# Kernel tuning notes

Hardware: AMD Instinct MI355X
Metric: run time of the kernel (lower is better)

Reference implementation:

```python
import jax, jax.numpy as jnp
import numpy as np

EMB = 2048
N_HEADS = 16
HEAD_DIM = 128
N_KV = 4
ROPE_BASE = 10000.0
B, S = 2, 2048


def _rope(x, cos, sin):
    # x: [B,S,h,d]; cos/sin: [1,S,1,d//2]
    x1, x2 = x[..., ::2], x[..., 1::2]
    return jnp.concatenate([x1 * cos - x2 * sin, x1 * sin + x2 * cos], axis=-1)


def setup_inputs() -> dict:
    key = jax.random.key(0)
    ks = jax.random.split(key, 5)
    x = jax.random.normal(ks[0], (B, S, EMB), dtype=jnp.float32)
    wq = jax.random.normal(ks[1], (EMB, N_HEADS * HEAD_DIM), dtype=jnp.float32) * 0.02
    wk = jax.random.normal(ks[2], (EMB, N_KV * HEAD_DIM), dtype=jnp.float32) * 0.02
    wv = jax.random.normal(ks[3], (EMB, N_KV * HEAD_DIM), dtype=jnp.float32) * 0.02
    wo = jax.random.normal(ks[4], (N_HEADS * HEAD_DIM, EMB), dtype=jnp.float32) * 0.02
    mask = jnp.tril(jnp.ones((S, S), dtype=bool))[None, None]  # [1,1,S,S] causal
    return {"x": x, "wq": wq, "wk": wk, "wv": wv, "wo": wo, "mask": mask}


def reference(x, wq, wk, wv, wo, mask):
    b, s, _ = x.shape
    q = (x @ wq).reshape(b, s, N_HEADS, HEAD_DIM)
    k = (x @ wk).reshape(b, s, N_KV, HEAD_DIM)
    v = (x @ wv).reshape(b, s, N_KV, HEAD_DIM)

    pos = jnp.arange(s, dtype=jnp.float32)
    dim_range = jnp.arange(0, HEAD_DIM, 2, dtype=jnp.float32)
    freqs = 1.0 / ROPE_BASE ** (dim_range / HEAD_DIM)
    angles = pos[:, None] * freqs[None, :]            # [S, d/2]
    cos = jnp.cos(angles)[None, :, None, :]           # [1,S,1,d/2]
    sin = jnp.sin(angles)[None, :, None, :]

    q = _rope(q, cos, sin)
    k = _rope(k, cos, sin)

    rep = N_HEADS // N_KV
    k = jnp.tile(k, (1, 1, rep, 1))  # matches torch .repeat on group dim
    v = jnp.tile(v, (1, 1, rep, 1))

    scale = 1.0 / jnp.sqrt(jnp.float32(HEAD_DIM))
    scores = jnp.einsum('bqhd,bkhd->bhqk', q, k) * scale  # [B,H,S,S]
    scores = jnp.where(mask, scores, -jnp.inf)
    attn = jax.nn.softmax(scores, axis=-1)  # dropout is identity in eval
    out = jnp.einsum('bhqk,bkhd->bqhd', attn, v).reshape(b, s, N_HEADS * HEAD_DIM)
    return out @ wo
```

## Files before the change

### kernel.cpp

```cpp
#include <hip/hip_runtime.h>

#define EMB 2048
#define NH 16
#define NKV 4
#define HD 128
#define SLEN 2048
#define BSZ 2
#define MROWS (BSZ * SLEN)

#define QOFF (BSZ * NH * SLEN * HD)
#define KOFF (BSZ * NKV * SLEN * HD)

typedef __attribute__((ext_vector_type(8))) short bf16x8;
typedef __attribute__((ext_vector_type(4))) float f32x4;
typedef __attribute__((ext_vector_type(2))) float f32x2;
typedef __attribute__((ext_vector_type(4))) short s16x4;

__device__ __forceinline__ short f2bf(float f) {
  union { float f; unsigned u; } v; v.f = f;
  unsigned r = (v.u + 0x7fffu + ((v.u >> 16) & 1u)) >> 16;
  return (short)r;
}

__global__ void rope_tab_k(f32x2* __restrict__ tab) {
  int i = blockIdx.x * blockDim.x + threadIdx.x;
  if (i >= SLEN * 64) return;
  int s = i >> 6, j = i & 63;
  float freq = exp2f(-(float)j * (13.287712379549449f / 64.0f));
  float ang = (float)s * freq;
  float sv, cv;
  sincosf(ang, &sv, &cv);
  f32x2 cs; cs[0] = cv; cs[1] = sv;
  tab[i] = cs;
}

__global__ void cast_bf16_k(const float* __restrict__ in, short* __restrict__ outp, int n) {
  int i = (blockIdx.x * blockDim.x + threadIdx.x) * 4;
  if (i >= n) return;
  f32x4 v = *(const f32x4*)(in + i);
  s16x4 r;
#pragma unroll
  for (int k = 0; k < 4; ++k) r[k] = f2bf(v[k]);
  *(s16x4*)(outp + i) = r;
}

__global__ void transpose_cast_k(const float* __restrict__ in, short* __restrict__ outp,
                                 int R, int C) {
  __shared__ float t[32][33];
  int c0 = blockIdx.x * 32, r0 = blockIdx.y * 32;
  int tx = threadIdx.x, ty = threadIdx.y;
#pragma unroll
  for (int i = 0; i < 4; ++i)
    t[ty + i * 8][tx] = in[(size_t)(r0 + ty + i * 8) * C + (c0 + tx)];
  __syncthreads();
#pragma unroll
  for (int i = 0; i < 4; ++i)
    outp[(size_t)(c0 + ty + i * 8) * R + (r0 + tx)] = f2bf(t[tx][ty + i * 8]);
}

#define BM 128
#define BN 128
#define BK 32

#define GLL16(g, l)                                                        \
  __builtin_amdgcn_global_load_lds(                                        \
      (const __attribute__((address_space(1))) void*)(g),                  \
      (__attribute__((address_space(3))) void*)(l), 16, 0, 0)

template <int EPI>
__global__ __launch_bounds__(256, 2) void gemm_bt_k(
    const short* __restrict__ A, const short* __restrict__ Bt,
    float* __restrict__ Cf, short* __restrict__ Cb,
    int M, int N, int K, const f32x2* __restrict__ rope) {
  __shared__ short lA[2][BM * BK];
  __shared__ short lB[2][BN * BK];
  int tid = threadIdx.x;
  int lane = tid & 63, wid = tid >> 6;
  int m0 = blockIdx.y * BM, n0 = blockIdx.x * BN;
  int wr = (wid >> 1) * 64, wc = (wid & 1) * 64;
  int l16 = lane & 15, lk = (lane >> 4) * 8;
  (void)M;

  auto stage = [&](int buf, int k0) {
    const short* ga = A + (size_t)m0 * K + k0;
    const short* gb = Bt + (size_t)n0 * K + k0;
#pragma unroll
    for (int i = 0; i < 2; ++i) {
      int cidx = i * 256 + tid;
      int row = cidx >> 2, c8 = (cidx & 3) << 3;
      GLL16(ga + (size_t)row * K + c8, &lA[buf][(size_t)(i * 256 + (tid & 192)) * 8]);
      GLL16(gb + (size_t)row * K + c8, &lB[buf][(size_t)(i * 256 + (tid & 192)) * 8]);
    }
  };

  f32x4 acc[4][4] = {};
  stage(0, 0);
  asm volatile("s_waitcnt vmcnt(0)" ::: "memory");
  __syncthreads();
  int nk = K / BK;
  for (int t = 0; t < nk; ++t) {
    int buf = t & 1;
    if (t + 1 < nk) stage(buf ^ 1, (t + 1) * BK);
    bf16x8 af[4], bfv[4];
#pragma unroll
    for (int m = 0; m < 4; ++m)
      af[m] = *(const bf16x8*)&lA[buf][(wr + m * 16 + l16) * BK + lk];
#pragma unroll
    for (int n = 0; n < 4; ++n)
      bfv[n] = *(const bf16x8*)&lB[buf][(wc + n * 16 + l16) * BK + lk];
#pragma unroll
    for (int m = 0; m < 4; ++m)
#pragma unroll
      for (int n = 0; n < 4; ++n)
        acc[m][n] = __builtin_amdgcn_mfma_f32_16x16x32_bf16(af[m], bfv[n], acc[m][n], 0, 0, 0);
    asm volatile("s_waitcnt vmcnt(0)" ::: "memory");
    __syncthreads();
  }

  const float SCL2E = 0.08838834764831845f * 1.4426950408889634f;
#pragma unroll
  for (int m = 0; m < 4; ++m) {
#pragma unroll
    for (int n = 0; n < 4; ++n) {
#pragma unroll
      for (int j = 0; j < 4; ++j) {
        int gm = m0 + wr + m * 16 + (lane >> 4) * 4 + j;
        int gc = n0 + wc + n * 16 + l16;
        float v = acc[m][n][j];
        if constexpr (EPI == 0) {
          Cf[(size_t)gm * N + gc] = v;
        } else {
          int pos = gm & (SLEN - 1), bb = gm >> 11;
          if (gc < 2560) {
            float p = __shfl_xor(v, 1);
            bool isq = gc < 2048;
            int gcc = isq ? gc : gc - 2048;
            int head = gcc >> 7, d = gcc & 127, j2 = d >> 1;
            f32x2 cs = rope[pos * 64 + j2];
            float ov; int od;
            if ((d & 1) == 0) { ov = v * cs[0] - p * cs[1]; od = j2; }
            else              { ov = p * cs[1] + v * cs[0]; od = j2 + 64; }
            if (isq) ov *= SCL2E;
            size_t idx = isq
                ? (((size_t)(bb * NH + head) * SLEN + pos) * HD + od)
                : ((size_t)QOFF + ((size_t)(bb * NKV + head) * SLEN + pos) * HD + od);
            Cb[idx] = f2bf(ov);
          } else {
            int gcc = gc - 2560;
            int head = gcc >> 7, d = gcc & 127;
            Cb[(size_t)QOFF + KOFF + ((size_t)(bb * NKV + head) * HD + d) * SLEN + pos] = f2bf(v);
          }
        }
      }
    }
  }
}

__global__ __launch_bounds__(512, 2) void flash_k(
    const short* __restrict__ Qb, const short* __restrict__ Kb,
    const short* __restrict__ Vt, short* __restrict__ O) {
  __shared__ short lK[4][64 * 128];
  __shared__ short lV[4][128 * 64];
  __shared__ short Plds[8][16][64];

  int tid = threadIdx.x, lane = tid & 63, wid = tid >> 6;
  int bh = blockIdx.y;
  int b = bh >> 4, h = bh & 15, kv = h & 3;
  int l16 = lane & 15, lk4 = lane >> 4;
  int qtA = 15 - (int)blockIdx.x;
  int qtB = (int)blockIdx.x;
  int ntA = 2 * (qtA + 1);
  int ntot = ntA + 2 * (qtB + 1);

  const short* qptr = Qb + (size_t)(b * NH + h) * SLEN * HD;
  const char* kg = (const char*)(Kb + (size_t)(b * NKV + kv) * SLEN * HD);
  const char* vg = (const char*)(Vt + (size_t)(b * NKV + kv) * HD * SLEN);

  int qbw = qtA * 128 + wid * 16;
  bf16x8 aq[4];
#pragma unroll
  for (int c = 0; c < 4; ++c)
    aq[c] = *(const bf16x8*)(qptr + (size_t)(qbw + l16) * HD + c * 32 + lk4 * 8);

  f32x4 o[8] = {};
  float m = -__builtin_inff();
  float lsum = 0.0f;

  char* myP = (char*)&Plds[wid][0][0];
  int swz = (l16 & 7) << 4;
  int swzk = l16 << 4;

  auto stageKV = [&](int buf, int k0) {
#pragma unroll
    for (int r = 0; r < 2; ++r) {
      int X = tid * 16 + r * 8192;
      int row = X >> 8, cb = X & 255;
      GLL16(kg + (size_t)(k0 + row) * 256 + (cb ^ ((row & 15) << 4)),
            (char*)&lK[buf][0] + X);
    }
#pragma unroll
    for (int r = 0; r < 2; ++r) {
      int X = tid * 16 + r * 8192;
      int row = X >> 7, cb = X & 127;
      GLL16(vg + (size_t)row * (SLEN * 2) + k0 * 2 + (cb ^ ((row & 7) << 4)),
            (char*)&lV[buf][0] + X);
    }
  };
  auto k0_of = [&](int t) { return (t < ntA ? t : t - ntA) * 64; };

  auto finalize = [&]() {
    float ls = lsum;
    ls += __shfl_xor(ls, 16);
    ls += __shfl_xor(ls, 32);
    float inv = 1.0f / ls;
    size_t ro = ((size_t)(b * SLEN + qbw + l16)) * (NH * HD) + h * HD;
#pragma unroll
    for (int dt = 0; dt < 8; ++dt) {
      s16x4 r;
#pragma unroll
      for (int j = 0; j < 4; ++j) r[j] = f2bf(o[dt][j] * inv);
      *(s16x4*)(O + ro + dt * 16 + lk4 * 4) = r;
    }
  };

  stageKV(0, k0_of(0));
  stageKV(1, k0_of(1));
  stageKV(2, k0_of(2));

  for (int tt = 0; tt < ntot; ++tt) {
    int rem = ntot - 1 - tt;
    if (rem >= 2)      asm volatile("s_waitcnt vmcnt(8)" ::: "memory");
    else if (rem == 1) asm volatile("s_waitcnt vmcnt(4)" ::: "memory");
    else               asm volatile("s_waitcnt vmcnt(0)" ::: "memory");
    __builtin_amdgcn_s_barrier();
    __builtin_amdgcn_sched_barrier(0);

    if (tt == ntA) {
      finalize();
#pragma unroll
      for (int dt = 0; dt < 8; ++dt) o[dt] = (f32x4){0.f, 0.f, 0.f, 0.f};
      m = -__builtin_inff();
      lsum = 0.0f;
      qbw = qtB * 128 + wid * 16;
#pragma unroll
      for (int c = 0; c < 4; ++c)
        aq[c] = *(const bf16x8*)(qptr + (size_t)(qbw + l16) * HD + c * 32 + lk4 * 8);
    }

    int k0 = k0_of(tt);
    int buf = tt & 3;
    if (k0 < qbw + 16) {
      const char* Kbase = (const char*)&lK[buf][0];
      const char* Vbase = (const char*)&lV[buf][0];
      f32x4 s[4] = {};
      __builtin_amdgcn_s_setprio(1);
#pragma unroll
      for (int c = 0; c < 4; ++c) {
#pragma unroll
        for (int t = 0; t < 4; ++t) {
          bf16x8 bk = *(const bf16x8*)(Kbase + (t * 16 + l16) * 256 + ((c * 64 + lk4 * 16) ^ swzk));
          s[t] = __builtin_amdgcn_mfma_f32_16x16x32_bf16(bk, aq[c], s[t], 0, 0, 0);
        }
      }
      __builtin_amdgcn_s_setprio(0);
      float x[16];
#pragma unroll
      for (int t = 0; t < 4; ++t)
#pragma unroll
        for (int j = 0; j < 4; ++j) x[t * 4 + j] = s[t][j];
      if (k0 + 63 > qbw) {
        int kq = k0 + lk4 * 4 - qbw - l16;
#pragma unroll
        for (int t = 0; t < 4; ++t)
#pragma unroll
          for (int j = 0; j < 4; ++j)
            if (kq + t * 16 + j > 0) x[t * 4 + j] = -3.0e38f;
      }
      float a0 = fmaxf(x[0], x[1]), a1 = fmaxf(x[2], x[3]);
      float a2 = fmaxf(x[4], x[5]), a3 = fmaxf(x[6], x[7]);
      float a4 = fmaxf(x[8], x[9]), a5 = fmaxf(x[10], x[11]);
      float a6 = fmaxf(x[12], x[13]), a7 = fmaxf(x[14], x[15]);
      float b0 = fmaxf(fmaxf(a0, a1), fmaxf(a2, a3));
      float b1 = fmaxf(fmaxf(a4, a5), fmaxf(a6, a7));
      float tm = fmaxf(b0, b1);
      tm = fmaxf(tm, __shfl_xor(tm, 16));
      tm = fmaxf(tm, __shfl_xor(tm, 32));
      float mn = fmaxf(m, tm);
      if (!__all(tm <= m + 8.0f)) {
        float f = __builtin_amdgcn_exp2f(m - mn);
        m = mn;
        lsum *= f;
#pragma unroll
        for (int dt = 0; dt < 8; ++dt) o[dt] *= f;
      }
      float psum = 0.0f;
#pragma unroll
      for (int t = 0; t < 4; ++t) {
        float p0 = __builtin_amdgcn_exp2f(x[t * 4 + 0] - m);
        float p1 = __builtin_amdgcn_exp2f(x[t * 4 + 1] - m);
        float p2 = __builtin_amdgcn_exp2f(x[t * 4 + 2] - m);
        float p3 = __builtin_amdgcn_exp2f(x[t * 4 + 3] - m);
        psum += (p0 + p1) + (p2 + p3);
        unsigned lo, hi;
        asm("v_cvt_pk_bf16_f32 %0, %1, %2" : "=v"(lo) : "v"(p0), "v"(p1));
        asm("v_cvt_pk_bf16_f32 %0, %1, %2" : "=v"(hi) : "v"(p2), "v"(p3));
        unsigned long long dw = ((unsigned long long)hi << 32) | lo;
        *(unsigned long long*)(myP + ((l16 * 128 + t * 32 + lk4 * 8) ^ swz)) = dw;
      }
      lsum += psum;
      asm volatile("s_waitcnt lgkmcnt(0)" ::: "memory");
      __builtin_amdgcn_sched_barrier(0);
      __builtin_amdgcn_s_setprio(1);
#pragma unroll
      for (int hh = 0; hh < 2; ++hh) {
        bf16x8 pa = *(const bf16x8*)(myP + ((l16 * 128 + hh * 64 + lk4 * 16) ^ swz));
#pragma unroll
        for (int dt = 0; dt < 8; ++dt) {
          bf16x8 bv = *(const bf16x8*)(Vbase + (dt * 16 + l16) * 128 + ((hh * 64 + lk4 * 16) ^ swz));
          o[dt] = __builtin_amdgcn_mfma_f32_16x16x32_bf16(bv, pa, o[dt], 0, 0, 0);
        }
      }
      __builtin_amdgcn_s_setprio(0);
    }
    if (tt + 3 < ntot) stageKV((tt + 3) & 3, k0_of(tt + 3));
  }
  finalize();
}

extern "C" void kernel_launch(void* const* d_in, const int* in_sizes, int n_in,
                              void* d_out, int out_size, void* d_ws, size_t ws_size,
                              hipStream_t stream) {
  const float* x  = (const float*)d_in[0];
  const float* wq = (const float*)d_in[1];
  const float* wk = (const float*)d_in[2];
  const float* wv = (const float*)d_in[3];
  const float* wo = (const float*)d_in[4];
  float* out = (float*)d_out;
  char* ws = (char*)d_ws;
  (void)in_sizes; (void)n_in; (void)out_size; (void)ws_size;

  const size_t MB = 1024 * 1024;
  f32x2* rope   = (f32x2*)(ws);
  short* xb     = (short*)(ws + 1 * MB);
  short* wqkvT  = (short*)(ws + 17 * MB);
  short* woT    = (short*)(ws + 29 * MB);
  short* QKVb   = (short*)(ws + 37 * MB);
  short* O      = xb;

  short* Qb = QKVb;
  short* Kb = QKVb + QOFF;
  short* Vt = QKVb + QOFF + KOFF;

  rope_tab_k<<<(SLEN * 64 + 255) / 256, 256, 0, stream>>>(rope);
  cast_bf16_k<<<(MROWS * EMB / 4 + 255) / 256, 256, 0, stream>>>(x, xb, MROWS * EMB);

  dim3 tb(32, 8);
  transpose_cast_k<<<dim3(2048 / 32, 2048 / 32), tb, 0, stream>>>(wq, wqkvT, 2048, 2048);
  transpose_cast_k<<<dim3(512 / 32, 2048 / 32), tb, 0, stream>>>(wk, wqkvT + 2048 * 2048, 2048, 512);
  transpose_cast_k<<<dim3(512 / 32, 2048 / 32), tb, 0, stream>>>(wv, wqkvT + 2560 * 2048, 2048, 512);
  transpose_cast_k<<<dim3(2048 / 32, 2048 / 32), tb, 0, stream>>>(wo, woT, 2048, 2048);

  gemm_bt_k<5><<<dim3(3072 / BN, MROWS / BM), 256, 0, stream>>>(xb, wqkvT, nullptr, QKVb, MROWS, 3072, 2048, rope);

  flash_k<<<dim3(8, BSZ * NH), 512, 0, stream>>>(Qb, Kb, Vt, O);

  gemm_bt_k<0><<<dim3(2048 / BN, MROWS / BM), 256, 0, stream>>>(O, woT, out, nullptr, MROWS, 2048, 2048, rope);
}
```

Baseline: 215.8 us.

## Use XOR-swizzled LDS tiles with BK=64 in the GEMM and raise MFMA priority

Doubles the GEMM K-tile to 64, halving the barrier and wait iterations per output tile. Stores A/B tiles in LDS with an XOR swizzle on 16-byte chunks to avoid bank conflicts on the fragment reads. Wraps each MFMA block in s_setprio so matrix work is issued ahead of other waves. It also drops the RoPE half-split reordering and writes Q/K in interleaved order, which is valid because the permutation is identical for Q and K. The larger tiles double LDS use per block, which may limit occupancy.

```diff
diff --git a/kernel.cpp b/kernel.cpp
--- a/kernel.cpp
+++ b/kernel.cpp
@@ -58,10 +58,6 @@
     outp[(size_t)(c0 + ty + i * 8) * R + (r0 + tx)] = f2bf(t[tx][ty + i * 8]);
 }
 
-#define BM 128
-#define BN 128
-#define BK 32
-
 #define GLL16(g, l)                                                        \
   __builtin_amdgcn_global_load_lds(                                        \
       (const __attribute__((address_space(1))) void*)(g),                  \
@@ -72,47 +68,60 @@
     const short* __restrict__ A, const short* __restrict__ Bt,
     float* __restrict__ Cf, short* __restrict__ Cb,
     int M, int N, int K, const f32x2* __restrict__ rope) {
-  __shared__ short lA[2][BM * BK];
-  __shared__ short lB[2][BN * BK];
+  __shared__ short lA[2][128 * 64];
+  __shared__ short lB[2][128 * 64];
   int tid = threadIdx.x;
   int lane = tid & 63, wid = tid >> 6;
-  int m0 = blockIdx.y * BM, n0 = blockIdx.x * BN;
+  int m0 = blockIdx.y * 128, n0 = blockIdx.x * 128;
   int wr = (wid >> 1) * 64, wc = (wid & 1) * 64;
-  int l16 = lane & 15, lk = (lane >> 4) * 8;
+  int l16 = lane & 15, lk4 = lane >> 4;
+  const int K2B = K * 2;
+  const char* Ab = (const char*)A;
+  const char* Bb = (const char*)Bt;
   (void)M;
 
   auto stage = [&](int buf, int k0) {
-    const short* ga = A + (size_t)m0 * K + k0;
-    const short* gb = Bt + (size_t)n0 * K + k0;
-#pragma unroll
-    for (int i = 0; i < 2; ++i) {
-      int cidx = i * 256 + tid;
-      int row = cidx >> 2, c8 = (cidx & 3) << 3;
-      GLL16(ga + (size_t)row * K + c8, &lA[buf][(size_t)(i * 256 + (tid & 192)) * 8]);
-      GLL16(gb + (size_t)row * K + c8, &lB[buf][(size_t)(i * 256 + (tid & 192)) * 8]);
-    }
+#pragma unroll
+    for (int r = 0; r < 4; ++r) {
+      int X = tid * 16 + r * 4096;
+      int row = X >> 7, cb = X & 127;
+      int logical = cb ^ ((row & 7) << 4);
+      GLL16(Ab + (size_t)(m0 + row) * K2B + k0 * 2 + logical, (char*)&lA[buf][0] + X);
+      GLL16(Bb + (size_t)(n0 + row) * K2B + k0 * 2 + logical, (char*)&lB[buf][0] + X);
+    }
+  };
+  auto ldA = [&](int buf, int m, int kk) {
+    int row = wr + m * 16 + l16;
+    return *(const bf16x8*)((char*)&lA[buf][0] + row * 128 + ((kk * 64 + lk4 * 16) ^ ((row & 7) << 4)));
+  };
+  auto ldB = [&](int buf, int n, int kk) {
+    int row = wc + n * 16 + l16;
+    return *(const bf16x8*)((char*)&lB[buf][0] + row * 128 + ((kk * 64 + lk4 * 16) ^ ((row & 7) << 4)));
   };
 
   f32x4 acc[4][4] = {};
   stage(0, 0);
   asm volatile("s_waitcnt vmcnt(0)" ::: "memory");
   __syncthreads();
-  int nk = K / BK;
+  int nk = K / 64;
   for (int t = 0; t < nk; ++t) {
     int buf = t & 1;
-    if (t + 1 < nk) stage(buf ^ 1, (t + 1) * BK);
-    bf16x8 af[4], bfv[4];
-#pragma unroll
-    for (int m = 0; m < 4; ++m)
-      af[m] = *(const bf16x8*)&lA[buf][(wr + m * 16 + l16) * BK + lk];
-#pragma unroll
-    for (int n = 0; n < 4; ++n)
-      bfv[n] = *(const bf16x8*)&lB[buf][(wc + n * 16 + l16) * BK + lk];
-#pragma unroll
-    for (int m = 0; m < 4; ++m)
-#pragma unroll
-      for (int n = 0; n < 4; ++n)
-        acc[m][n] = __builtin_amdgcn_mfma_f32_16x16x32_bf16(af[m], bfv[n], acc[m][n], 0, 0, 0);
+    if (t + 1 < nk) stage(buf ^ 1, (t + 1) * 64);
+#pragma unroll
+    for (int kk = 0; kk < 2; ++kk) {
+      bf16x8 af[4], bfv[4];
+#pragma unroll
+      for (int m = 0; m < 4; ++m) af[m] = ldA(buf, m, kk);
+#pragma unroll
+      for (int n = 0; n < 4; ++n) bfv[n] = ldB(buf, n, kk);
+      __builtin_amdgcn_s_setprio(1);
+#pragma unroll
+      for (int m = 0; m < 4; ++m)
+#pragma unroll
+        for (int n = 0; n < 4; ++n)
+          acc[m][n] = __builtin_amdgcn_mfma_f32_16x16x32_bf16(af[m], bfv[n], acc[m][n], 0, 0, 0);
+      __builtin_amdgcn_s_setprio(0);
+    }
     asm volatile("s_waitcnt vmcnt(0)" ::: "memory");
     __syncthreads();
   }
@@ -124,7 +133,7 @@
     for (int n = 0; n < 4; ++n) {
 #pragma unroll
       for (int j = 0; j < 4; ++j) {
-        int gm = m0 + wr + m * 16 + (lane >> 4) * 4 + j;
+        int gm = m0 + wr + m * 16 + lk4 * 4 + j;
         int gc = n0 + wc + n * 16 + l16;
         float v = acc[m][n][j];
         if constexpr (EPI == 0) {
@@ -135,15 +144,14 @@
             float p = __shfl_xor(v, 1);
             bool isq = gc < 2048;
             int gcc = isq ? gc : gc - 2048;
-            int head = gcc >> 7, d = gcc & 127, j2 = d >> 1;
-            f32x2 cs = rope[pos * 64 + j2];
-            float ov; int od;
-            if ((d & 1) == 0) { ov = v * cs[0] - p * cs[1]; od = j2; }
-            else              { ov = p * cs[1] + v * cs[0]; od = j2 + 64; }
+            int head = gcc >> 7, d = gcc & 127;
+            f32x2 cs = rope[pos * 64 + (d >> 1)];
+            float ov = ((d & 1) == 0) ? (v * cs[0] - p * cs[1])
+                                      : (p * cs[1] + v * cs[0]);
             if (isq) ov *= SCL2E;
             size_t idx = isq
-                ? (((size_t)(bb * NH + head) * SLEN + pos) * HD + od)
-                : ((size_t)QOFF + ((size_t)(bb * NKV + head) * SLEN + pos) * HD + od);
+                ? (((size_t)(bb * NH + head) * SLEN + pos) * HD + d)
+                : ((size_t)QOFF + ((size_t)(bb * NKV + head) * SLEN + pos) * HD + d);
             Cb[idx] = f2bf(ov);
           } else {
             int gcc = gc - 2560;
@@ -360,9 +368,9 @@
   transpose_cast_k<<<dim3(512 / 32, 2048 / 32), tb, 0, stream>>>(wv, wqkvT + 2560 * 2048, 2048, 512);
   transpose_cast_k<<<dim3(2048 / 32, 2048 / 32), tb, 0, stream>>>(wo, woT, 2048, 2048);
 
-  gemm_bt_k<5><<<dim3(3072 / BN, MROWS / BM), 256, 0, stream>>>(xb, wqkvT, nullptr, QKVb, MROWS, 3072, 2048, rope);
+  gemm_bt_k<5><<<dim3(3072 / 128, MROWS / 128), 256, 0, stream>>>(xb, wqkvT, nullptr, QKVb, MROWS, 3072, 2048, rope);
 
   flash_k<<<dim3(8, BSZ * NH), 512, 0, stream>>>(Qb, Kb, Vt, O);
 
-  gemm_bt_k<0><<<dim3(2048 / BN, MROWS / BM), 256, 0, stream>>>(O, woT, out, nullptr, MROWS, 2048, 2048, rope);
-}
+  gemm_bt_k<0><<<dim3(2048 / 128, MROWS / 128), 256, 0, stream>>>(O, woT, out, nullptr, MROWS, 2048, 2048, rope);
+}
```

Result: slower. 225.7 us (+4.6%).
